# Kernel optimization log

Measured on AMD Instinct MI355X. Metric: run time of the kernel, lower is better.

The kernel has to match this reference:

```python
import jax, jax.numpy as jnp
import numpy as np

D = 1024
H = 16
HD = D // H
FF = 4096
B, N = 8, 1024


def setup_inputs() -> dict:
    key = jax.random.key(0)
    ks = jax.random.split(key, 12)
    s = lambda fan_in: 1.0 / np.sqrt(fan_in)
    return {
        "x": jax.random.normal(ks[0], (B, N, D), dtype=jnp.float32),
        "ln1_g": jnp.ones((D,), jnp.float32),
        "ln1_b": jnp.zeros((D,), jnp.float32),
        "ln2_g": jnp.ones((D,), jnp.float32),
        "ln2_b": jnp.zeros((D,), jnp.float32),
        "W_qkv": jax.random.uniform(ks[1], (3 * D, D), jnp.float32, -s(D), s(D)),
        "b_qkv": jax.random.uniform(ks[2], (3 * D,), jnp.float32, -s(D), s(D)),
        "W_proj": jax.random.uniform(ks[3], (D, D), jnp.float32, -s(D), s(D)),
        "b_proj": jax.random.uniform(ks[4], (D,), jnp.float32, -s(D), s(D)),
        "W1": jax.random.uniform(ks[5], (FF, D), jnp.float32, -s(D), s(D)),
        "b1": jax.random.uniform(ks[6], (FF,), jnp.float32, -s(D), s(D)),
        "W2": jax.random.uniform(ks[7], (D, FF), jnp.float32, -s(FF), s(FF)),
        "b2": jax.random.uniform(ks[8], (D,), jnp.float32, -s(FF), s(FF)),
    }


def _layernorm(x, g, b, eps=1e-5):
    mu = jnp.mean(x, axis=-1, keepdims=True)
    var = jnp.mean(jnp.square(x - mu), axis=-1, keepdims=True)
    return (x - mu) * jax.lax.rsqrt(var + eps) * g + b


def _gelu(x):
    return jax.nn.gelu(x, approximate=False)  # torch nn.GELU default (erf)


def _forward(x, ln1_g, ln1_b, ln2_g, ln2_b, W_qkv, b_qkv, W_proj, b_proj, W1, b1, W2, b2):
    b, n, d = x.shape
    h = _layernorm(x, ln1_g, ln1_b)
    qkv = h @ W_qkv.T + b_qkv                      # [B,N,3D]
    qkv = qkv.reshape(b, n, 3, H, HD).transpose(2, 0, 3, 1, 4)  # [3,B,H,N,HD]
    q, k, v = qkv[0], qkv[1], qkv[2]
    scores = jnp.einsum("bhqd,bhkd->bhqk", q, k) / np.sqrt(HD)
    attn = jax.nn.softmax(scores, axis=-1)
    ctx = jnp.einsum("bhqk,bhkd->bhqd", attn, v)   # [B,H,N,HD]
    ctx = ctx.transpose(0, 2, 1, 3).reshape(b, n, d)
    attn_out = ctx @ W_proj.T + b_proj
    out = attn_out + x                              # residual 1
    skip = out
    hh = _layernorm(out, ln2_g, ln2_b)
    hh = _gelu(hh @ W1.T + b1)
    hh = _gelu(hh @ W2.T + b2)                      # note: final GELU per source
    return hh + skip


def reference(x, ln1_g, ln1_b, ln2_g, ln2_b, W_qkv, b_qkv, W_proj, b_proj, W1, b1, W2, b2):
    return _forward(x, ln1_g, ln1_b, ln2_g, ln2_b, W_qkv, b_qkv, W_proj, b_proj, W1, b1, W2, b2)
```

## Files before the change

### kernel.cpp

```cpp
#include <hip/hip_runtime.h>


typedef unsigned short ushort_t;
typedef __bf16 bf16x8 __attribute__((ext_vector_type(8)));
typedef float f32x4 __attribute__((ext_vector_type(4)));
typedef unsigned short u16x8 __attribute__((ext_vector_type(8)));

__device__ __forceinline__ void async_ld16(const void* g, void* l) {
  __builtin_amdgcn_global_load_lds(
      (void __attribute__((address_space(1)))*)const_cast<void*>(g),
      (void __attribute__((address_space(3)))*)l, 16, 0, 0);
}

__device__ __forceinline__ float bf2f(ushort_t h) {
  union { unsigned int u; float f; } v;
  v.u = ((unsigned int)h) << 16;
  return v.f;
}
__device__ __forceinline__ ushort_t f2bf(float f) {
  union { float f; unsigned int u; } v;
  v.f = f;
  unsigned int r = v.u + 0x7FFFu + ((v.u >> 16) & 1u);
  return (ushort_t)(r >> 16);
}
__device__ __forceinline__ float gelu_f(float x) {
  float y = 0.7978845608028654f * (x + 0.044715f * x * x * x);
  float e = __expf(2.0f * y);
  float t = 1.0f - 2.0f / (e + 1.0f);
  return 0.5f * x * (1.0f + t);
}

__global__ void __launch_bounds__(256) cvt_f32_bf16(const float* __restrict__ src,
                                                    ushort_t* __restrict__ dst, int n) {
  int i = (blockIdx.x * 256 + threadIdx.x) * 8;
  if (i >= n) return;
  float4 a = *(const float4*)(src + i);
  float4 b = *(const float4*)(src + i + 4);
  u16x8 o;
  o[0] = f2bf(a.x); o[1] = f2bf(a.y); o[2] = f2bf(a.z); o[3] = f2bf(a.w);
  o[4] = f2bf(b.x); o[5] = f2bf(b.y); o[6] = f2bf(b.z); o[7] = f2bf(b.w);
  *(u16x8*)(dst + i) = o;
}

__global__ void __launch_bounds__(256) ln_f32(const float* __restrict__ X,
                                              const float* __restrict__ G,
                                              const float* __restrict__ Bb,
                                              ushort_t* __restrict__ Y) {
  int tok = blockIdx.x * 4 + (threadIdx.x >> 6);
  int lane = threadIdx.x & 63;
  const float* xr = X + (size_t)tok * 1024 + lane * 16;
  float v[16];
#pragma unroll
  for (int c = 0; c < 4; c++) {
    float4 a = *(const float4*)(xr + c * 4);
    v[c * 4 + 0] = a.x; v[c * 4 + 1] = a.y; v[c * 4 + 2] = a.z; v[c * 4 + 3] = a.w;
  }
  float s = 0.f, ss = 0.f;
#pragma unroll
  for (int j = 0; j < 16; j++) { s += v[j]; ss += v[j] * v[j]; }
#pragma unroll
  for (int off = 32; off >= 1; off >>= 1) {
    s += __shfl_xor(s, off);
    ss += __shfl_xor(ss, off);
  }
  float mu = s * (1.f / 1024.f);
  float var = ss * (1.f / 1024.f) - mu * mu;
  float rs = rsqrtf(var + 1e-5f);
  u16x8 o0, o1;
#pragma unroll
  for (int c = 0; c < 4; c++) {
    float4 g = *(const float4*)(G + lane * 16 + c * 4);
    float4 bb = *(const float4*)(Bb + lane * 16 + c * 4);
    ushort_t* op = (c < 2) ? (ushort_t*)&o0 : (ushort_t*)&o1;
    int base = (c & 1) * 4;
    op[base + 0] = f2bf((v[c * 4 + 0] - mu) * rs * g.x + bb.x);
    op[base + 1] = f2bf((v[c * 4 + 1] - mu) * rs * g.y + bb.y);
    op[base + 2] = f2bf((v[c * 4 + 2] - mu) * rs * g.z + bb.z);
    op[base + 3] = f2bf((v[c * 4 + 3] - mu) * rs * g.w + bb.w);
  }
  ushort_t* yr = Y + (size_t)tok * 1024 + lane * 16;
  *(u16x8*)yr = o0;
  *(u16x8*)(yr + 8) = o1;
}

__global__ void __launch_bounds__(256) ln_bf16(const ushort_t* __restrict__ X,
                                               const float* __restrict__ G,
                                               const float* __restrict__ Bb,
                                               ushort_t* __restrict__ Y) {
  int tok = blockIdx.x * 4 + (threadIdx.x >> 6);
  int lane = threadIdx.x & 63;
  const ushort_t* xr = X + (size_t)tok * 1024 + lane * 16;
  u16x8 x0 = *(const u16x8*)xr;
  u16x8 x1 = *(const u16x8*)(xr + 8);
  float v[16];
  float s = 0.f, ss = 0.f;
#pragma unroll
  for (int j = 0; j < 8; j++) { v[j] = bf2f(x0[j]); v[8 + j] = bf2f(x1[j]); }
#pragma unroll
  for (int j = 0; j < 16; j++) { s += v[j]; ss += v[j] * v[j]; }
#pragma unroll
  for (int off = 32; off >= 1; off >>= 1) {
    s += __shfl_xor(s, off);
    ss += __shfl_xor(ss, off);
  }
  float mu = s * (1.f / 1024.f);
  float var = ss * (1.f / 1024.f) - mu * mu;
  float rs = rsqrtf(var + 1e-5f);
  u16x8 o0, o1;
#pragma unroll
  for (int c = 0; c < 4; c++) {
    float4 g = *(const float4*)(G + lane * 16 + c * 4);
    float4 bb = *(const float4*)(Bb + lane * 16 + c * 4);
    ushort_t* op = (c < 2) ? (ushort_t*)&o0 : (ushort_t*)&o1;
    int base = (c & 1) * 4;
    op[base + 0] = f2bf((v[c * 4 + 0] - mu) * rs * g.x + bb.x);
    op[base + 1] = f2bf((v[c * 4 + 1] - mu) * rs * g.y + bb.y);
    op[base + 2] = f2bf((v[c * 4 + 2] - mu) * rs * g.z + bb.z);
    op[base + 3] = f2bf((v[c * 4 + 3] - mu) * rs * g.w + bb.w);
  }
  ushort_t* yr = Y + (size_t)tok * 1024 + lane * 16;
  *(u16x8*)yr = o0;
  *(u16x8*)(yr + 8) = o1;
}

template <int BK>
__global__ void __launch_bounds__(256, (BK == 64 ? 4 : 2))
gemm_bt(const ushort_t* __restrict__ A,
        const ushort_t* __restrict__ Bw,
        const float* __restrict__ bias,
        const float* __restrict__ ResF,
        const ushort_t* __restrict__ ResB,
        ushort_t* __restrict__ Cb,
        float* __restrict__ Cf,
        int M, int N, int K, int act, int swz) {
  constexpr int NG = BK / 8;
  constexpr int GM = NG - 1;
  constexpr int RPP = 2048 / BK;
  constexpr int NP = BK / 16;
  constexpr int NC = BK / 32;
  __shared__ __align__(16) ushort_t sAB[2 * 128 * BK];
  ushort_t* sA = sAB;
  ushort_t* sB = sAB + 128 * BK;
  int t = threadIdx.x;
  int wave = t >> 6, lane = t & 63;
  int quad = lane >> 4, l16 = lane & 15;
  int wm = (wave & 1) * 64, wn = (wave >> 1) * 64;

  int bx = blockIdx.x, by = blockIdx.y;
  if (swz) {
    int lid = by * gridDim.x + bx;
    int xcd = lid & 7, slot = lid >> 3;
    int mchunk = gridDim.y >> 3;
    by = xcd * mchunk + slot / gridDim.x;
    bx = slot % gridDim.x;
  }
  int m0 = by * 128, n0 = bx * 128;

  f32x4 zero = {0.f, 0.f, 0.f, 0.f};
  f32x4 acc[4][4];
#pragma unroll
  for (int i = 0; i < 4; i++)
#pragma unroll
    for (int j = 0; j < 4; j++) acc[i][j] = zero;

  int srow = t / NG;
  int scol = ((t & GM) ^ (srow & GM)) * 8;
  const ushort_t* gA = A + (size_t)(m0 + srow) * K + scol;
  const ushort_t* gB = Bw + (size_t)(n0 + srow) * K + scol;

  for (int k0 = 0; k0 < K; k0 += BK) {
#pragma unroll
    for (int p = 0; p < NP; p++) {
      async_ld16(gA + (size_t)p * RPP * K + k0, sA + p * 2048 + wave * 512);
      async_ld16(gB + (size_t)p * RPP * K + k0, sB + p * 2048 + wave * 512);
    }
    __syncthreads();
#pragma unroll
    for (int c = 0; c < NC; c++) {
      int col = (((c * 4 + quad) ^ (l16 & GM)) * 8);
      bf16x8 af[4], bfr[4];
#pragma unroll
      for (int i = 0; i < 4; i++) {
        af[i]  = *(const bf16x8*)(sA + (wm + i * 16 + l16) * BK + col);
        bfr[i] = *(const bf16x8*)(sB + (wn + i * 16 + l16) * BK + col);
      }
#pragma unroll
      for (int mi = 0; mi < 4; mi++)
#pragma unroll
        for (int ni = 0; ni < 4; ni++)
          acc[mi][ni] = __builtin_amdgcn_mfma_f32_16x16x32_bf16(af[mi], bfr[ni], acc[mi][ni], 0, 0, 0);
    }
    __syncthreads();
  }

  float bv[4];
#pragma unroll
  for (int ni = 0; ni < 4; ni++) bv[ni] = bias[n0 + wn + ni * 16 + l16];

  if (Cf) {
#pragma unroll
    for (int mi = 0; mi < 4; mi++) {
      int row = m0 + wm + mi * 16 + quad * 4;
#pragma unroll
      for (int ni = 0; ni < 4; ni++) {
        int col = n0 + wn + ni * 16 + l16;
#pragma unroll
        for (int r = 0; r < 4; r++) {
          size_t idx = (size_t)(row + r) * N + col;
          float vv = acc[mi][ni][r] + bv[ni];
          if (act) vv = gelu_f(vv);
          if (ResB) vv += bf2f(ResB[idx]);
          Cf[idx] = vv;
        }
      }
    }
  } else {
    ushort_t* eb = sAB + wave * (16 * 72);
    int lr = lane >> 2, lc = (lane & 3) * 8;
#pragma unroll
    for (int mi = 0; mi < 4; mi++) {
      int row = m0 + wm + mi * 16;
#pragma unroll
      for (int ni = 0; ni < 4; ni++)
#pragma unroll
        for (int r = 0; r < 4; r++) {
          float vv = acc[mi][ni][r] + bv[ni];
          if (act) vv = gelu_f(vv);
          eb[(quad * 4 + r) * 72 + ni * 16 + l16] = f2bf(vv);
        }
#pragma unroll
      for (int hc = 0; hc < 64; hc += 32) {
        u16x8 o = *(const u16x8*)(eb + lr * 72 + hc + lc);
        size_t gidx = (size_t)(row + lr) * N + n0 + wn + hc + lc;
        if (ResF) {
          float4 ra = *(const float4*)(ResF + gidx);
          float4 rb = *(const float4*)(ResF + gidx + 4);
          u16x8 o2;
          o2[0] = f2bf(bf2f(o[0]) + ra.x); o2[1] = f2bf(bf2f(o[1]) + ra.y);
          o2[2] = f2bf(bf2f(o[2]) + ra.z); o2[3] = f2bf(bf2f(o[3]) + ra.w);
          o2[4] = f2bf(bf2f(o[4]) + rb.x); o2[5] = f2bf(bf2f(o[5]) + rb.y);
          o2[6] = f2bf(bf2f(o[6]) + rb.z); o2[7] = f2bf(bf2f(o[7]) + rb.w);
          *(u16x8*)(Cb + gidx) = o2;
        } else {
          *(u16x8*)(Cb + gidx) = o;
        }
      }
    }
  }
}

__global__ void __launch_bounds__(256) vtrans(const ushort_t* __restrict__ qkv,
                                              ushort_t* __restrict__ Vt) {
  __shared__ ushort_t tile[64][72];
  int t = threadIdx.x;
  int bh = blockIdx.y;
  int b = bh >> 4, h = bh & 15;
  int n0 = blockIdx.x * 64;
  int r = t >> 3;
  int c8 = (t & 7) * 8;
  const ushort_t* src = qkv + ((size_t)(b * 1024 + n0)) * 3072 + 2048 + h * 64;
#pragma unroll
  for (int rr = r; rr < 64; rr += 32) {
    u16x8 d = *(const u16x8*)(src + (size_t)rr * 3072 + c8);
#pragma unroll
    for (int j = 0; j < 8; j++) tile[rr][c8 + j] = d[j];
  }
  __syncthreads();
#pragma unroll
  for (int hh = r; hh < 64; hh += 32) {
    u16x8 o;
#pragma unroll
    for (int j = 0; j < 8; j++) o[j] = tile[c8 + j][hh];
    *(u16x8*)(Vt + ((size_t)bh * 64 + hh) * 1024 + n0 + c8) = o;
  }
}

__global__ void __launch_bounds__(256) attn_kernel(const ushort_t* __restrict__ qkv,
                                                   const ushort_t* __restrict__ Vt,
                                                   ushort_t* __restrict__ ctx) {
  __shared__ __align__(16) ushort_t sK[128 * 64];
  __shared__ __align__(16) ushort_t sV[64 * 128];
  __shared__ __align__(16) ushort_t sP[4 * 16 * 144];
  int t = threadIdx.x, wave = t >> 6, lane = t & 63;
  int quad = lane >> 4, l16 = lane & 15;
  int bh = blockIdx.y, b = bh >> 4, h = bh & 15;
  int q0 = blockIdx.x * 64 + wave * 16;
  size_t tokbase = (size_t)b * 1024;

  const ushort_t* qrow = qkv + (tokbase + q0 + l16) * 3072 + h * 64;
  bf16x8 qf0 = *(const bf16x8*)(qrow + quad * 8);
  bf16x8 qf1 = *(const bf16x8*)(qrow + 32 + quad * 8);

  f32x4 zero = {0.f, 0.f, 0.f, 0.f};
  f32x4 O[4];
#pragma unroll
  for (int i = 0; i < 4; i++) O[i] = zero;
  float m = -3.0e38f, l = 0.f;

  int kvlK = wave * 32 + (lane >> 3);
  int hdKx = lane & 7;
  ushort_t* pw = sP + wave * (16 * 144);

  for (int kv0 = 0; kv0 < 1024; kv0 += 128) {
#pragma unroll
    for (int j = 0; j < 4; j++) {
      int kvl = kvlK + j * 8;
      int hd = (hdKx ^ (kvl & 7)) * 8;
      async_ld16(qkv + (tokbase + kv0 + kvl) * 3072 + 1024 + h * 64 + hd,
                 sK + wave * 2048 + j * 512);
      int hdv = wave * 16 + j * 4 + (lane >> 4);
      int kvloc = ((lane & 15) ^ (hdv & 15)) * 8;
      async_ld16(Vt + ((size_t)bh * 64 + hdv) * 1024 + kv0 + kvloc,
                 sV + wave * 2048 + j * 512);
    }
    __syncthreads();

    f32x4 st[8];
#pragma unroll
    for (int s = 0; s < 8; s++) {
      bf16x8 kf0 = *(const bf16x8*)(sK + (s * 16 + l16) * 64 + ((quad ^ (l16 & 7)) * 8));
      bf16x8 kf1 = *(const bf16x8*)(sK + (s * 16 + l16) * 64 + (((4 + quad) ^ (l16 & 7)) * 8));
      st[s] = __builtin_amdgcn_mfma_f32_16x16x32_bf16(kf0, qf0, zero, 0, 0, 0);
      st[s] = __builtin_amdgcn_mfma_f32_16x16x32_bf16(kf1, qf1, st[s], 0, 0, 0);
    }
    f32x4 mx4 = st[0];
#pragma unroll
    for (int s = 1; s < 8; s++)
#pragma unroll
      for (int r = 0; r < 4; r++) mx4[r] = fmaxf(mx4[r], st[s][r]);
    float mx = fmaxf(fmaxf(mx4[0], mx4[1]), fmaxf(mx4[2], mx4[3]));
    mx = fmaxf(mx, __shfl_xor(mx, 16));
    mx = fmaxf(mx, __shfl_xor(mx, 32));
    float mnew = fmaxf(m, mx * 0.125f);
    float alpha = __expf(m - mnew);
    m = mnew;
    float rs = 0.f;
#pragma unroll
    for (int s = 0; s < 8; s++)
#pragma unroll
      for (int r = 0; r < 4; r++) {
        st[s][r] = __expf(fmaf(st[s][r], 0.125f, -m));
        rs += st[s][r];
      }
    rs += __shfl_xor(rs, 16);
    rs += __shfl_xor(rs, 32);
    l = l * alpha + rs;
#pragma unroll
    for (int s = 0; s < 8; s++) {
      uint2 pk;
      pk.x = __builtin_amdgcn_perm(__float_as_uint(st[s][1]), __float_as_uint(st[s][0]), 0x07060302u);
      pk.y = __builtin_amdgcn_perm(__float_as_uint(st[s][3]), __float_as_uint(st[s][2]), 0x07060302u);
      *(uint2*)(pw + l16 * 144 + s * 16 + quad * 4) = pk;
    }
#pragma unroll
    for (int ti = 0; ti < 4; ti++)
#pragma unroll
      for (int r = 0; r < 4; r++) O[ti][r] *= alpha;
#pragma unroll
    for (int c = 0; c < 4; c++) {
      bf16x8 pf = *(const bf16x8*)(pw + l16 * 144 + c * 32 + quad * 8);
#pragma unroll
      for (int ti = 0; ti < 4; ti++) {
        bf16x8 vf = *(const bf16x8*)(sV + (ti * 16 + l16) * 128 + (((c * 4 + quad) ^ l16) * 8));
        O[ti] = __builtin_amdgcn_mfma_f32_16x16x32_bf16(vf, pf, O[ti], 0, 0, 0);
      }
    }
    __syncthreads();
  }
  float inv = 1.0f / l;
  ushort_t* cb = ctx + (tokbase + q0 + l16) * 1024 + h * 64;
#pragma unroll
  for (int ti = 0; ti < 4; ti++) {
    uint2 pk;
    pk.x = (unsigned int)f2bf(O[ti][0] * inv) | ((unsigned int)f2bf(O[ti][1] * inv) << 16);
    pk.y = (unsigned int)f2bf(O[ti][2] * inv) | ((unsigned int)f2bf(O[ti][3] * inv) << 16);
    *(uint2*)(cb + ti * 16 + quad * 4) = pk;
  }
}

extern "C" void kernel_launch(void* const* d_in, const int* in_sizes, int n_in,
                              void* d_out, int out_size, void* d_ws, size_t ws_size,
                              hipStream_t stream) {
  (void)in_sizes; (void)n_in; (void)out_size; (void)ws_size;
  const float* x     = (const float*)d_in[0];
  const float* ln1g  = (const float*)d_in[1];
  const float* ln1b  = (const float*)d_in[2];
  const float* ln2g  = (const float*)d_in[3];
  const float* ln2b  = (const float*)d_in[4];
  const float* Wqkv  = (const float*)d_in[5];
  const float* bqkv  = (const float*)d_in[6];
  const float* Wproj = (const float*)d_in[7];
  const float* bproj = (const float*)d_in[8];
  const float* W1    = (const float*)d_in[9];
  const float* b1    = (const float*)d_in[10];
  const float* W2    = (const float*)d_in[11];
  const float* b2    = (const float*)d_in[12];
  float* out = (float*)d_out;
  char* ws = (char*)d_ws;
  const size_t MB = 1u << 20;
  ushort_t* Wqkv_b  = (ushort_t*)(ws + 0);
  ushort_t* Wproj_b = (ushort_t*)(ws + 6 * MB);
  ushort_t* h1      = (ushort_t*)(ws + 8 * MB);
  ushort_t* qkv     = (ushort_t*)(ws + 24 * MB);
  ushort_t* Vt      = (ushort_t*)(ws + 72 * MB);
  ushort_t* ctx     = (ushort_t*)(ws + 8 * MB);
  ushort_t* out1    = (ushort_t*)(ws + 24 * MB);
  ushort_t* W1_b    = (ushort_t*)(ws + 0);
  ushort_t* h2      = (ushort_t*)(ws + 8 * MB);
  ushort_t* ff1     = (ushort_t*)(ws + 40 * MB);
  ushort_t* W2_b    = (ushort_t*)(ws + 0);

  cvt_f32_bf16<<<1536, 256, 0, stream>>>(Wqkv, Wqkv_b, 3 * 1024 * 1024);
  cvt_f32_bf16<<<512, 256, 0, stream>>>(Wproj, Wproj_b, 1024 * 1024);
  ln_f32<<<2048, 256, 0, stream>>>(x, ln1g, ln1b, h1);
  gemm_bt<64><<<dim3(24, 64), 256, 0, stream>>>(h1, Wqkv_b, bqkv, nullptr, nullptr, qkv, nullptr, 8192, 3072, 1024, 0, 0);
  vtrans<<<dim3(16, 128), 256, 0, stream>>>(qkv, Vt);
  attn_kernel<<<dim3(16, 128), 256, 0, stream>>>(qkv, Vt, ctx);
  gemm_bt<128><<<dim3(8, 64), 256, 0, stream>>>(ctx, Wproj_b, bproj, x, nullptr, out1, nullptr, 8192, 1024, 1024, 0, 0);
  cvt_f32_bf16<<<2048, 256, 0, stream>>>(W1, W1_b, 4 * 1024 * 1024);
  ln_bf16<<<2048, 256, 0, stream>>>(out1, ln2g, ln2b, h2);
  gemm_bt<64><<<dim3(32, 64), 256, 0, stream>>>(h2, W1_b, b1, nullptr, nullptr, ff1, nullptr, 8192, 4096, 1024, 1, 0);
  cvt_f32_bf16<<<2048, 256, 0, stream>>>(W2, W2_b, 4 * 1024 * 1024);
  gemm_bt<128><<<dim3(8, 64), 256, 0, stream>>>(ff1, W2_b, b2, nullptr, out1, nullptr, out, 8192, 1024, 4096, 1, 1);
}
```

Baseline: 506.7 us.

## Tune attention softmax with exp2, lazy rescale, setprio; merge weight conversions

The attention softmax now works in base 2 with a folded scale constant and uses a hardware exp2 builtin. The running max and the O rescale are updated only when some lane's new max exceeds the old one by more than 8, which skips multiplies on most iterations. The P scratch row stride changes from 144 to 152 to alter LDS bank mapping, and wave priority is raised around the MFMA sections. The two weight conversion launches are merged into one kernel to save a launch. The lazy rescale lets unnormalised exponentials grow up to 2^8, which narrows bf16 precision headroom.

```diff
diff --git a/kernel.cpp b/kernel.cpp
--- a/kernel.cpp
+++ b/kernel.cpp
@@ -22,6 +22,13 @@
   v.f = f;
   unsigned int r = v.u + 0x7FFFu + ((v.u >> 16) & 1u);
   return (ushort_t)(r >> 16);
+}
+__device__ __forceinline__ float fast_exp2(float x) {
+#if __has_builtin(__builtin_amdgcn_exp2f)
+  return __builtin_amdgcn_exp2f(x);
+#else
+  return __expf(x * 0.6931471805599453f);
+#endif
 }
 __device__ __forceinline__ float gelu_f(float x) {
   float y = 0.7978845608028654f * (x + 0.044715f * x * x * x);
@@ -40,6 +47,28 @@
   o[0] = f2bf(a.x); o[1] = f2bf(a.y); o[2] = f2bf(a.z); o[3] = f2bf(a.w);
   o[4] = f2bf(b.x); o[5] = f2bf(b.y); o[6] = f2bf(b.z); o[7] = f2bf(b.w);
   *(u16x8*)(dst + i) = o;
+}
+
+__global__ void __launch_bounds__(256) cvt_f32_bf16_2(const float* __restrict__ s0,
+                                                      ushort_t* __restrict__ d0, int n0,
+                                                      const float* __restrict__ s1,
+                                                      ushort_t* __restrict__ d1, int n1) {
+  int i = (blockIdx.x * 256 + threadIdx.x) * 8;
+  const float* src;
+  ushort_t* dst;
+  if (i < n0) {
+    src = s0 + i; dst = d0 + i;
+  } else {
+    int j = i - n0;
+    if (j >= n1) return;
+    src = s1 + j; dst = d1 + j;
+  }
+  float4 a = *(const float4*)(src);
+  float4 b = *(const float4*)(src + 4);
+  u16x8 o;
+  o[0] = f2bf(a.x); o[1] = f2bf(a.y); o[2] = f2bf(a.z); o[3] = f2bf(a.w);
+  o[4] = f2bf(b.x); o[5] = f2bf(b.y); o[6] = f2bf(b.z); o[7] = f2bf(b.w);
+  *(u16x8*)dst = o;
 }
 
 __global__ void __launch_bounds__(256) ln_f32(const float* __restrict__ X,
@@ -280,12 +309,13 @@
                                                    ushort_t* __restrict__ ctx) {
   __shared__ __align__(16) ushort_t sK[128 * 64];
   __shared__ __align__(16) ushort_t sV[64 * 128];
-  __shared__ __align__(16) ushort_t sP[4 * 16 * 144];
+  __shared__ __align__(16) ushort_t sP[4 * 16 * 152];
   int t = threadIdx.x, wave = t >> 6, lane = t & 63;
   int quad = lane >> 4, l16 = lane & 15;
   int bh = blockIdx.y, b = bh >> 4, h = bh & 15;
   int q0 = blockIdx.x * 64 + wave * 16;
   size_t tokbase = (size_t)b * 1024;
+  const float SC2 = 0.18033688011112042f;
 
   const ushort_t* qrow = qkv + (tokbase + q0 + l16) * 3072 + h * 64;
   bf16x8 qf0 = *(const bf16x8*)(qrow + quad * 8);
@@ -295,11 +325,11 @@
   f32x4 O[4];
 #pragma unroll
   for (int i = 0; i < 4; i++) O[i] = zero;
-  float m = -3.0e38f, l = 0.f;
+  float m2 = -3.0e38f, l = 0.f;
 
   int kvlK = wave * 32 + (lane >> 3);
   int hdKx = lane & 7;
-  ushort_t* pw = sP + wave * (16 * 144);
+  ushort_t* pw = sP + wave * (16 * 152);
 
   for (int kv0 = 0; kv0 < 1024; kv0 += 128) {
 #pragma unroll
@@ -316,6 +346,7 @@
     __syncthreads();
 
     f32x4 st[8];
+    __builtin_amdgcn_s_setprio(1);
 #pragma unroll
     for (int s = 0; s < 8; s++) {
       bf16x8 kf0 = *(const bf16x8*)(sK + (s * 16 + l16) * 64 + ((quad ^ (l16 & 7)) * 8));
@@ -323,6 +354,7 @@
       st[s] = __builtin_amdgcn_mfma_f32_16x16x32_bf16(kf0, qf0, zero, 0, 0, 0);
       st[s] = __builtin_amdgcn_mfma_f32_16x16x32_bf16(kf1, qf1, st[s], 0, 0, 0);
     }
+    __builtin_amdgcn_s_setprio(0);
     f32x4 mx4 = st[0];
 #pragma unroll
     for (int s = 1; s < 8; s++)
@@ -331,40 +363,46 @@
     float mx = fmaxf(fmaxf(mx4[0], mx4[1]), fmaxf(mx4[2], mx4[3]));
     mx = fmaxf(mx, __shfl_xor(mx, 16));
     mx = fmaxf(mx, __shfl_xor(mx, 32));
-    float mnew = fmaxf(m, mx * 0.125f);
-    float alpha = __expf(m - mnew);
-    m = mnew;
+    float mx2 = mx * SC2;
+    if (!__all(mx2 - m2 <= 8.0f)) {
+      float mnew2 = fmaxf(m2, mx2);
+      float alpha = fast_exp2(m2 - mnew2);
+      m2 = mnew2;
+      l *= alpha;
+#pragma unroll
+      for (int ti = 0; ti < 4; ti++)
+#pragma unroll
+        for (int r = 0; r < 4; r++) O[ti][r] *= alpha;
+    }
     float rs = 0.f;
 #pragma unroll
     for (int s = 0; s < 8; s++)
 #pragma unroll
       for (int r = 0; r < 4; r++) {
-        st[s][r] = __expf(fmaf(st[s][r], 0.125f, -m));
+        st[s][r] = fast_exp2(fmaf(st[s][r], SC2, -m2));
         rs += st[s][r];
       }
     rs += __shfl_xor(rs, 16);
     rs += __shfl_xor(rs, 32);
-    l = l * alpha + rs;
+    l += rs;
 #pragma unroll
     for (int s = 0; s < 8; s++) {
       uint2 pk;
       pk.x = __builtin_amdgcn_perm(__float_as_uint(st[s][1]), __float_as_uint(st[s][0]), 0x07060302u);
       pk.y = __builtin_amdgcn_perm(__float_as_uint(st[s][3]), __float_as_uint(st[s][2]), 0x07060302u);
-      *(uint2*)(pw + l16 * 144 + s * 16 + quad * 4) = pk;
-    }
-#pragma unroll
-    for (int ti = 0; ti < 4; ti++)
-#pragma unroll
-      for (int r = 0; r < 4; r++) O[ti][r] *= alpha;
+      *(uint2*)(pw + l16 * 152 + s * 16 + quad * 4) = pk;
+    }
+    __builtin_amdgcn_s_setprio(1);
 #pragma unroll
     for (int c = 0; c < 4; c++) {
-      bf16x8 pf = *(const bf16x8*)(pw + l16 * 144 + c * 32 + quad * 8);
+      bf16x8 pf = *(const bf16x8*)(pw + l16 * 152 + c * 32 + quad * 8);
 #pragma unroll
       for (int ti = 0; ti < 4; ti++) {
         bf16x8 vf = *(const bf16x8*)(sV + (ti * 16 + l16) * 128 + (((c * 4 + quad) ^ l16) * 8));
         O[ti] = __builtin_amdgcn_mfma_f32_16x16x32_bf16(vf, pf, O[ti], 0, 0, 0);
       }
     }
+    __builtin_amdgcn_s_setprio(0);
     __syncthreads();
   }
   float inv = 1.0f / l;
@@ -410,8 +448,8 @@
   ushort_t* ff1     = (ushort_t*)(ws + 40 * MB);
   ushort_t* W2_b    = (ushort_t*)(ws + 0);
 
-  cvt_f32_bf16<<<1536, 256, 0, stream>>>(Wqkv, Wqkv_b, 3 * 1024 * 1024);
-  cvt_f32_bf16<<<512, 256, 0, stream>>>(Wproj, Wproj_b, 1024 * 1024);
+  cvt_f32_bf16_2<<<2048, 256, 0, stream>>>(Wqkv, Wqkv_b, 3 * 1024 * 1024,
+                                           Wproj, Wproj_b, 1024 * 1024);
   ln_f32<<<2048, 256, 0, stream>>>(x, ln1g, ln1b, h1);
   gemm_bt<64><<<dim3(24, 64), 256, 0, stream>>>(h1, Wqkv_b, bqkv, nullptr, nullptr, qkv, nullptr, 8192, 3072, 1024, 0, 0);
   vtrans<<<dim3(16, 128), 256, 0, stream>>>(qkv, Vt);
```

Result: faster. 476.9 us (-5.9%).
